# Optimization experiments

Measured on AMD Instinct MI355X. Metric: run time of the kernel, lower is better.

The kernel has to match this reference:

```python
import jax, jax.numpy as jnp
import numpy as np

B, C, H, W = 16, 256, 128, 128
INTER = C // 2  # NLBlockND default inter_channels = in_channels // 2
BN_EPS = 1e-5


def setup_inputs() -> dict:
    key = jax.random.key(0)
    ks = jax.random.split(key, 14)
    s = lambda n: 1.0 / np.sqrt(n)
    inp = {
        'x':  jax.random.normal(ks[0], (B, C, H, W), jnp.float32),
        # NLBlockND 1x1 convs (spatial input is 1x1 after avg-pool -> matmuls)
        'Wg': jax.random.normal(ks[1], (INTER, C), jnp.float32) * s(C),
        'bg': jax.random.normal(ks[2], (INTER,), jnp.float32) * s(C),
        'Wt': jax.random.normal(ks[3], (INTER, C), jnp.float32) * s(C),
        'bt': jax.random.normal(ks[4], (INTER,), jnp.float32) * s(C),
        'Wp': jax.random.normal(ks[5], (INTER, C), jnp.float32) * s(C),
        'bp': jax.random.normal(ks[6], (INTER,), jnp.float32) * s(C),
        'Wf': jax.random.normal(ks[7], (1, 2 * INTER), jnp.float32) * s(2 * INTER),
        'bf': jax.random.normal(ks[8], (1,), jnp.float32) * s(2 * INTER),
        'Wz': jax.random.normal(ks[9], (C, INTER), jnp.float32) * s(INTER),
        'bz': jax.random.normal(ks[10], (C,), jnp.float32) * s(INTER),
        'gamma': jax.random.normal(ks[11], (C,), jnp.float32),
        'beta':  jax.random.normal(ks[12], (C,), jnp.float32),
        # eca_layer_two: Conv2d(C, 1, kernel_size=1, bias=False)
        'W3': jax.random.normal(ks[13], (1, C), jnp.float32) * s(C),
    }
    return inp


def reference(x, Wg, bg, Wt, bt, Wp, bp, Wf, bf, Wz, bz, gamma, beta, W3):
    b = x.shape[0]
    # ---- nonlocal_layer: avg-pool -> NLBlockND('concatenate') on 1x1 map ----
    p = jnp.mean(x, axis=(2, 3))                      # [b, C] pooled vector
    g_x = p @ Wg.T + bg                               # [b, INTER]
    th  = p @ Wt.T + bt                               # theta  [b, INTER]
    ph  = p @ Wp.T + bp                               # phi    [b, INTER]
    cat = jnp.concatenate([th, ph], axis=1)           # [b, 2*INTER]
    f = jax.nn.relu(cat @ Wf.T + bf)                  # [b, 1]; N=1 so f_div_C = f
    y = f * g_x                                       # [b, INTER]
    wy = y @ Wz.T + bz                                # [b, C]
    # BatchNorm2d (training mode, spatial=1x1): stats over batch per channel
    mu = jnp.mean(wy, axis=0)
    var = jnp.var(wy, axis=0)
    bn = gamma * (wy - mu) * jax.lax.rsqrt(var + BN_EPS) + beta
    z = bn + p                                        # residual
    scores = jax.nn.sigmoid(z)                        # [b, C]
    # top-3 channel selection, then per-sample gather of channels from x
    _, idx = jax.lax.top_k(scores, 3)                 # [b, 3]
    x1 = jnp.take_along_axis(x, idx[:, :, None, None], axis=1)  # [b, 3, H, W]
    # ---- eca_layer_two: 1x1 conv C->1 (no bias) + exact GELU ----
    x3 = jax.nn.gelu(jnp.einsum('bchw,oc->bohw', x, W3), approximate=False)  # [b,1,H,W]
    # conv2 (eca_layer_one) output is discarded (x2 = zeros_like, unused)
    return jnp.concatenate([x3, x1], axis=1)          # [b, 4, H, W]
```

## Files before the change

kernel.cpp:

```cpp
#include <hip/hip_runtime.h>

#define HW    16384
#define NCH   256
#define NB    16
#define INTER 128
#define HW4   4096


__global__ __launch_bounds__(256) void k_pool_x3(
    const float* __restrict__ x, const float* __restrict__ W3, float* out)
{
    const int tile = blockIdx.x;
    const int b    = blockIdx.y;
    const int tid  = threadIdx.x;
    const int wave = tid >> 6, lane = tid & 63;

    __shared__ float w3f[NCH];
    __shared__ float wsum[4][NCH];
    w3f[tid] = W3[tid];
    __syncthreads();

    const int p4 = tile * 256 + tid;
    const float4* xb = (const float4*)x + (size_t)b * NCH * HW4 + p4;

    float4 bufA[8], bufB[8];
    float a0 = 0.f, a1 = 0.f, a2 = 0.f, a3 = 0.f;

    #pragma unroll
    for (int j = 0; j < 8; ++j) bufA[j] = xb[(size_t)j * HW4];

    #define PROCESS(BUF, CBASE)                                             \
        _Pragma("unroll")                                                   \
        for (int j = 0; j < 8; ++j) {                                       \
            const int c = (CBASE) + j;                                      \
            float4 v = BUF[j];                                              \
            float w = w3f[c];                                               \
            a0 = fmaf(v.x, w, a0); a1 = fmaf(v.y, w, a1);                   \
            a2 = fmaf(v.z, w, a2); a3 = fmaf(v.w, w, a3);                   \
            float cs = (v.x + v.y) + (v.z + v.w);                           \
            cs += __shfl_xor(cs, 1);                                        \
            cs += __shfl_xor(cs, 2);                                        \
            cs += __shfl_xor(cs, 4);                                        \
            cs += __shfl_xor(cs, 8);                                        \
            cs += __shfl_xor(cs, 16);                                       \
            cs += __shfl_xor(cs, 32);                                       \
            if (lane == 0) wsum[wave][c] = cs;                              \
        }

    for (int cb = 0; cb < 32; cb += 2) {
        #pragma unroll
        for (int j = 0; j < 8; ++j) bufB[j] = xb[(size_t)((cb + 1) * 8 + j) * HW4];
        PROCESS(bufA, cb * 8)
        if (cb + 2 < 32) {
            #pragma unroll
            for (int j = 0; j < 8; ++j) bufA[j] = xb[(size_t)((cb + 2) * 8 + j) * HW4];
        }
        PROCESS(bufB, (cb + 1) * 8)
    }
    #undef PROCESS

    __syncthreads();
    float s = wsum[0][tid] + wsum[1][tid] + wsum[2][tid] + wsum[3][tid];
    out[(size_t)(b * 4 + 1) * HW + tile * NCH + tid] = s;

    const float is2 = 0.70710678118654752440f;
    float4 g;
    g.x = 0.5f * a0 * (1.f + erff(a0 * is2));
    g.y = 0.5f * a1 * (1.f + erff(a1 * is2));
    g.z = 0.5f * a2 * (1.f + erff(a2 * is2));
    g.w = 0.5f * a3 * (1.f + erff(a3 * is2));
    ((float4*)out)[(size_t)b * 4 * HW4 + p4] = g;
}

__global__ __launch_bounds__(256) void k_mlp(
    const float* outbuf,
    const float* __restrict__ Wg, const float* __restrict__ bg,
    const float* __restrict__ Wt, const float* __restrict__ bt,
    const float* __restrict__ Wp, const float* __restrict__ bp,
    const float* __restrict__ Wf, const float* __restrict__ bfv,
    const float* __restrict__ Wz, const float* __restrict__ bz,
    float* __restrict__ p_out, float* __restrict__ wy_out)
{
    const int b = blockIdx.x, tid = threadIdx.x;
    __shared__ float sp[NCH];
    __shared__ float sg[INTER], sth[INTER], sph[INTER];
    __shared__ float red[NCH];
    __shared__ float sy[INTER];
    __shared__ float sf;

    const float* psum = outbuf + (size_t)(b * 4 + 1) * HW;
    float s = 0.f;
    #pragma unroll
    for (int t = 0; t < 16; ++t) s += psum[t * NCH + tid];
    float pv = s * (1.0f / 16384.0f);
    sp[tid] = pv;
    p_out[b * NCH + tid] = pv;
    __syncthreads();

    for (int j = tid; j < 3 * INTER; j += 256) {
        const float* Wrow; float bias; int i, which;
        if (j < INTER)        { i = j;           Wrow = Wg + i * NCH; bias = bg[i]; which = 0; }
        else if (j < 2*INTER) { i = j - INTER;   Wrow = Wt + i * NCH; bias = bt[i]; which = 1; }
        else                  { i = j - 2*INTER; Wrow = Wp + i * NCH; bias = bp[i]; which = 2; }
        float acc = bias;
        for (int k = 0; k < NCH; k += 4) {
            float4 q = *(const float4*)(Wrow + k);
            acc = fmaf(q.x, sp[k+0], acc);
            acc = fmaf(q.y, sp[k+1], acc);
            acc = fmaf(q.z, sp[k+2], acc);
            acc = fmaf(q.w, sp[k+3], acc);
        }
        if (which == 0) sg[i] = acc;
        else if (which == 1) sth[i] = acc;
        else sph[i] = acc;
    }
    __syncthreads();

    float cat = (tid < INTER) ? sth[tid] : sph[tid - INTER];
    red[tid] = cat * Wf[tid];
    __syncthreads();
    if (tid == 0) {
        float acc = bfv[0];
        for (int k = 0; k < NCH; ++k) acc += red[k];
        sf = fmaxf(acc, 0.f);
    }
    __syncthreads();
    if (tid < INTER) sy[tid] = sf * sg[tid];
    __syncthreads();

    {
        const float* Wrow = Wz + tid * INTER;
        float acc = bz[tid];
        for (int k = 0; k < INTER; k += 4) {
            float4 q = *(const float4*)(Wrow + k);
            acc = fmaf(q.x, sy[k+0], acc);
            acc = fmaf(q.y, sy[k+1], acc);
            acc = fmaf(q.z, sy[k+2], acc);
            acc = fmaf(q.w, sy[k+3], acc);
        }
        wy_out[b * NCH + tid] = acc;
    }
}

__global__ __launch_bounds__(256) void k_bn_topk(
    const float* __restrict__ wy, const float* __restrict__ p,
    const float* __restrict__ gamma, const float* __restrict__ beta,
    int* __restrict__ sel_out)
{
    const int b = blockIdx.x, tid = threadIdx.x;
    const int wave = tid >> 6, lane = tid & 63;
    __shared__ float wsc[4];
    __shared__ int   wid[4];
    __shared__ int   sel[3];

    float vv[16];
    float mu = 0.f;
    #pragma unroll
    for (int bb = 0; bb < 16; ++bb) { vv[bb] = wy[bb * NCH + tid]; mu += vv[bb]; }
    mu *= (1.f / 16.f);
    float var = 0.f;
    #pragma unroll
    for (int bb = 0; bb < 16; ++bb) { float d = vv[bb] - mu; var = fmaf(d, d, var); }
    var *= (1.f / 16.f);

    float bn = gamma[tid] * (vv[b] - mu) * rsqrtf(var + 1e-5f) + beta[tid];
    float z  = bn + p[b * NCH + tid];
    float sc = 1.f / (1.f + expf(-z));

    for (int r = 0; r < 3; ++r) {
        float s = sc; int id = tid;
        #pragma unroll
        for (int m = 1; m <= 32; m <<= 1) {
            float so = __shfl_xor(s, m);
            int   io = __shfl_xor(id, m);
            if (so > s || (so == s && io < id)) { s = so; id = io; }
        }
        if (lane == 0) { wsc[wave] = s; wid[wave] = id; }
        __syncthreads();
        if (tid == 0) {
            float bs = wsc[0]; int bi = wid[0];
            for (int w = 1; w < 4; ++w)
                if (wsc[w] > bs || (wsc[w] == bs && wid[w] < bi)) { bs = wsc[w]; bi = wid[w]; }
            sel[r] = bi;
        }
        __syncthreads();
        if (tid == sel[r]) sc = -1e30f;
        __syncthreads();
    }
    if (tid < 3) sel_out[b * 3 + tid] = sel[tid];
}

__global__ __launch_bounds__(256) void k_gather(
    const float* __restrict__ x, const int* __restrict__ sel,
    float* __restrict__ out)
{
    const int seg = blockIdx.x;
    const int r   = blockIdx.y;
    const int b   = blockIdx.z;
    const int ch  = sel[b * 3 + r];
    const float4* src = (const float4*)x + (size_t)(b * NCH + ch) * HW4 + seg * 1024;
    float4*       dst = (float4*)out + (size_t)(b * 4 + 1 + r) * HW4 + seg * 1024;
    #pragma unroll
    for (int i = 0; i < 4; ++i)
        dst[i * 256 + threadIdx.x] = src[i * 256 + threadIdx.x];
}

extern "C" void kernel_launch(void* const* d_in, const int* in_sizes, int n_in,
                              void* d_out, int out_size, void* d_ws, size_t ws_size,
                              hipStream_t stream)
{
    const float* x     = (const float*)d_in[0];
    const float* Wg    = (const float*)d_in[1];
    const float* bg    = (const float*)d_in[2];
    const float* Wt    = (const float*)d_in[3];
    const float* bt    = (const float*)d_in[4];
    const float* Wp    = (const float*)d_in[5];
    const float* bp    = (const float*)d_in[6];
    const float* Wf    = (const float*)d_in[7];
    const float* bfv   = (const float*)d_in[8];
    const float* Wz    = (const float*)d_in[9];
    const float* bz    = (const float*)d_in[10];
    const float* gamma = (const float*)d_in[11];
    const float* beta  = (const float*)d_in[12];
    const float* W3    = (const float*)d_in[13];
    float* out = (float*)d_out;

    float* wy  = (float*)d_ws;
    float* p   = wy + NB * NCH;
    int*   sel = (int*)(p + NB * NCH);

    k_pool_x3<<<dim3(16, 16), 256, 0, stream>>>(x, W3, out);
    k_mlp<<<NB, 256, 0, stream>>>(out, Wg, bg, Wt, bt, Wp, bp, Wf, bfv, Wz, bz, p, wy);
    k_bn_topk<<<NB, 256, 0, stream>>>(wy, p, gamma, beta, sel);
    k_gather<<<dim3(4, 3, NB), 256, 0, stream>>>(x, sel, out);
}
```

Baseline: 419.3 us.

## Split pooling kernel into more smaller blocks and use DPP wave reductions

The pooling/x3 kernel now launches 1024 blocks of 128 threads, each thread handling a float2 instead of a float4, so more waves are in flight for the streaming read of x. The per-channel wave sum replaces six `__shfl_xor` exchanges with a DPP row-shift and row-broadcast sequence whose total lands in lane 63. Per-tile partial sums grow from 16 to 64 per channel. They are stored in the scratch region of the output and summed in the MLP kernel. The tradeoff is narrower loads and four times as many partials to reduce.

```diff
diff --git a/kernel.cpp b/kernel.cpp
--- a/kernel.cpp
+++ b/kernel.cpp
@@ -4,10 +4,29 @@
 #define NCH   256
 #define NB    16
 #define INTER 128
+#define HW2   8192
 #define HW4   4096
 
 
-__global__ __launch_bounds__(256) void k_pool_x3(
+__device__ __forceinline__ float wave_sum64(float x) {
+    int v = __float_as_int(x);
+    int t;
+    t = __builtin_amdgcn_update_dpp(0, v, 0x111, 0xf, 0xf, true);
+    v = __float_as_int(__int_as_float(v) + __int_as_float(t));
+    t = __builtin_amdgcn_update_dpp(0, v, 0x112, 0xf, 0xf, true);
+    v = __float_as_int(__int_as_float(v) + __int_as_float(t));
+    t = __builtin_amdgcn_update_dpp(0, v, 0x114, 0xf, 0xf, true);
+    v = __float_as_int(__int_as_float(v) + __int_as_float(t));
+    t = __builtin_amdgcn_update_dpp(0, v, 0x118, 0xf, 0xf, true);
+    v = __float_as_int(__int_as_float(v) + __int_as_float(t));
+    t = __builtin_amdgcn_update_dpp(0, v, 0x142, 0xa, 0xf, true);
+    v = __float_as_int(__int_as_float(v) + __int_as_float(t));
+    t = __builtin_amdgcn_update_dpp(0, v, 0x143, 0xc, 0xf, true);
+    v = __float_as_int(__int_as_float(v) + __int_as_float(t));
+    return __int_as_float(v);
+}
+
+__global__ __launch_bounds__(128) void k_pool_x3(
     const float* __restrict__ x, const float* __restrict__ W3, float* out)
 {
     const int tile = blockIdx.x;
@@ -16,60 +35,53 @@
     const int wave = tid >> 6, lane = tid & 63;
 
     __shared__ float w3f[NCH];
-    __shared__ float wsum[4][NCH];
-    w3f[tid] = W3[tid];
-    __syncthreads();
-
-    const int p4 = tile * 256 + tid;
-    const float4* xb = (const float4*)x + (size_t)b * NCH * HW4 + p4;
-
-    float4 bufA[8], bufB[8];
-    float a0 = 0.f, a1 = 0.f, a2 = 0.f, a3 = 0.f;
-
-    #pragma unroll
-    for (int j = 0; j < 8; ++j) bufA[j] = xb[(size_t)j * HW4];
+    __shared__ float wsum[2][NCH];
+    w3f[tid]       = W3[tid];
+    w3f[tid + 128] = W3[tid + 128];
+    __syncthreads();
+
+    const int p2 = tile * 128 + tid;
+    const float2* xb = (const float2*)x + (size_t)b * NCH * HW2 + p2;
+
+    float2 bufA[8], bufB[8];
+    float a0 = 0.f, a1 = 0.f;
+
+    #pragma unroll
+    for (int j = 0; j < 8; ++j) bufA[j] = xb[(size_t)j * HW2];
 
     #define PROCESS(BUF, CBASE)                                             \
         _Pragma("unroll")                                                   \
         for (int j = 0; j < 8; ++j) {                                       \
             const int c = (CBASE) + j;                                      \
-            float4 v = BUF[j];                                              \
+            float2 v = BUF[j];                                              \
             float w = w3f[c];                                               \
             a0 = fmaf(v.x, w, a0); a1 = fmaf(v.y, w, a1);                   \
-            a2 = fmaf(v.z, w, a2); a3 = fmaf(v.w, w, a3);                   \
-            float cs = (v.x + v.y) + (v.z + v.w);                           \
-            cs += __shfl_xor(cs, 1);                                        \
-            cs += __shfl_xor(cs, 2);                                        \
-            cs += __shfl_xor(cs, 4);                                        \
-            cs += __shfl_xor(cs, 8);                                        \
-            cs += __shfl_xor(cs, 16);                                       \
-            cs += __shfl_xor(cs, 32);                                       \
-            if (lane == 0) wsum[wave][c] = cs;                              \
+            float cs = wave_sum64(v.x + v.y);                               \
+            if (lane == 63) wsum[wave][c] = cs;                             \
         }
 
     for (int cb = 0; cb < 32; cb += 2) {
         #pragma unroll
-        for (int j = 0; j < 8; ++j) bufB[j] = xb[(size_t)((cb + 1) * 8 + j) * HW4];
+        for (int j = 0; j < 8; ++j) bufB[j] = xb[(size_t)((cb + 1) * 8 + j) * HW2];
         PROCESS(bufA, cb * 8)
         if (cb + 2 < 32) {
             #pragma unroll
-            for (int j = 0; j < 8; ++j) bufA[j] = xb[(size_t)((cb + 2) * 8 + j) * HW4];
+            for (int j = 0; j < 8; ++j) bufA[j] = xb[(size_t)((cb + 2) * 8 + j) * HW2];
         }
         PROCESS(bufB, (cb + 1) * 8)
     }
     #undef PROCESS
 
     __syncthreads();
-    float s = wsum[0][tid] + wsum[1][tid] + wsum[2][tid] + wsum[3][tid];
-    out[(size_t)(b * 4 + 1) * HW + tile * NCH + tid] = s;
+    float* ps = out + (size_t)(b * 4 + 1) * HW + tile * NCH;
+    ps[tid]       = wsum[0][tid]       + wsum[1][tid];
+    ps[tid + 128] = wsum[0][tid + 128] + wsum[1][tid + 128];
 
     const float is2 = 0.70710678118654752440f;
-    float4 g;
+    float2 g;
     g.x = 0.5f * a0 * (1.f + erff(a0 * is2));
     g.y = 0.5f * a1 * (1.f + erff(a1 * is2));
-    g.z = 0.5f * a2 * (1.f + erff(a2 * is2));
-    g.w = 0.5f * a3 * (1.f + erff(a3 * is2));
-    ((float4*)out)[(size_t)b * 4 * HW4 + p4] = g;
+    ((float2*)out)[(size_t)b * 4 * HW2 + p2] = g;
 }
 
 __global__ __launch_bounds__(256) void k_mlp(
@@ -91,7 +103,7 @@
     const float* psum = outbuf + (size_t)(b * 4 + 1) * HW;
     float s = 0.f;
     #pragma unroll
-    for (int t = 0; t < 16; ++t) s += psum[t * NCH + tid];
+    for (int t = 0; t < 64; ++t) s += psum[t * NCH + tid];
     float pv = s * (1.0f / 16384.0f);
     sp[tid] = pv;
     p_out[b * NCH + tid] = pv;
@@ -229,7 +241,7 @@
     float* p   = wy + NB * NCH;
     int*   sel = (int*)(p + NB * NCH);
 
-    k_pool_x3<<<dim3(16, 16), 256, 0, stream>>>(x, W3, out);
+    k_pool_x3<<<dim3(64, 16), 128, 0, stream>>>(x, W3, out);
     k_mlp<<<NB, 256, 0, stream>>>(out, Wg, bg, Wt, bt, Wp, bp, Wf, bfv, Wz, bz, p, wy);
     k_bn_topk<<<NB, 256, 0, stream>>>(wy, p, gamma, beta, sel);
     k_gather<<<dim3(4, 3, NB), 256, 0, stream>>>(x, sel, out);
```

New measurement: 423.2 us. No clear change (+0.9%).
